# Optimization experiments

Measured on AMD Instinct MI355X. Metric: run time of the kernel, lower is better.

The kernel has to match this reference:

```python
import jax, jax.numpy as jnp
import numpy as np

N, E, G, H, L = 50000, 400000, 2000, 128, 5
NPG = N // G  # 25 nodes per graph
EPS = 1e-5    # PNA std epsilon
D_LOG = 1.0   # avg_d['log'] as in 3DInfomax PNAGNN


def setup_inputs():
    key = jax.random.key(0)
    ks = jax.random.split(key, 32)
    node_feat = jax.random.randint(ks[0], (N, 9), 0, 16)
    edge_feat = jax.random.randint(ks[1], (E, 3), 0, 5)
    src = jax.random.randint(ks[2], (E,), 0, N)
    off = jax.random.randint(ks[3], (E,), 1, NPG)
    # dst stays in the same graph as src and differs from src
    dst = (src // NPG) * NPG + (src % NPG + off) % NPG
    graph_id = jnp.arange(N) // NPG
    inp = dict(node_feat=node_feat, edge_feat=edge_feat, src=src, dst=dst,
               graph_id=graph_id)
    shapes = [("aemb_f", (144, H)), ("bemb_f", (15, H)),
              ("w_pre_f", (L, 3 * H, H)), ("b_pre_f", (L, H)),
              ("w_post_f", (L, 13 * H, H)), ("b_post_f", (L, H)),
              ("w_out3", (3 * H, 256)), ("b_out3", (256,)),
              ("aemb", (144, H)), ("bemb", (15, H)),
              ("w_pre", (L, 3 * H, H)), ("b_pre", (L, H)),
              ("w_post", (L, 13 * H, H)), ("b_post", (L, H)),
              ("w1", (3 * H + 256, H)), ("b1", (H,)),
              ("w2", (H, 128)), ("b2", (128,))]
    for i, (n, s) in enumerate(shapes):
        inp[n] = jax.random.normal(ks[4 + i], s, dtype=jnp.float32) * 0.05
    return inp


def _embed(table, x, vocab):
    # sum of per-feature embeddings (OGB Atom/Bond encoder)
    idx = x + jnp.arange(x.shape[1]) * vocab
    return table[idx].sum(axis=1)


def _pna_gnn(aemb, bemb, w_pre, b_pre, w_post, b_post,
             node_feat, edge_feat, src, dst):
    h = _embed(aemb, node_feat, 16)   # [N, H]
    e = _embed(bemb, edge_feat, 5)    # [E, H]
    deg = jax.ops.segment_sum(jnp.ones((src.shape[0],), jnp.float32), dst, N)
    safe_deg = jnp.maximum(deg, 1.0)[:, None]
    log_deg = jnp.log(deg + 1.0)[:, None]
    amp = log_deg / D_LOG                                   # amplification scaler
    att = jnp.where(log_deg > 0, D_LOG / jnp.where(log_deg > 0, log_deg, 1.0), 0.0)
    has_in = (deg > 0)[:, None]
    for l in range(L):
        h_in = h
        # pretrans over edges: cat(src, dst, edge) -> linear (pretrans_layers=1, last_activation='none')
        z = jnp.concatenate([h[src], h[dst], e], axis=-1) @ w_pre[l] + b_pre[l]  # [E, H]
        s1 = jax.ops.segment_sum(z, dst, N)
        mean = s1 / safe_deg
        mean_sq = jax.ops.segment_sum(z * z, dst, N) / safe_deg
        std = jnp.sqrt(jax.nn.relu(mean_sq - mean * mean) + EPS)
        mx = jnp.where(has_in, jax.ops.segment_max(z, dst, N), 0.0)
        mn = jnp.where(has_in, jax.ops.segment_min(z, dst, N), 0.0)
        agg = jnp.concatenate([mean, mx, mn, std], axis=-1)          # [N, 4H]
        f = jnp.concatenate([agg, agg * amp, agg * att], axis=-1)    # [N, 12H]
        f = jnp.where(has_in, f, 0.0)  # DGL leaves zero-in-degree nodes at zero
        h = jnp.concatenate([h, f], axis=-1) @ w_post[l] + b_post[l]
        h = h + h_in  # residual
    return h


def _readout(h, graph_id):
    mean = jax.ops.segment_sum(h, graph_id, G) / NPG
    mx = jax.ops.segment_max(h, graph_id, G)
    mn = jax.ops.segment_min(h, graph_id, G)
    return jnp.concatenate([mn, mx, mean], axis=-1)  # order: min, max, mean


def reference(aemb_f, bemb_f, w_pre_f, b_pre_f, w_post_f, b_post_f,
              w_out3, b_out3, aemb, bemb, w_pre, b_pre, w_post, b_post,
              w1, b1, w2, b2, node_feat, edge_feat, src, dst, graph_id):
    # frozen 3D branch (torch.no_grad + detach -> stop_gradient)
    h3 = _pna_gnn(aemb_f, bemb_f, w_pre_f, b_pre_f, w_post_f, b_post_f,
                  node_feat, edge_feat, src, dst)
    r3 = _readout(h3, graph_id)
    latent3d = jax.lax.stop_gradient(r3 @ w_out3 + b_out3)  # [G, 256]
    # trainable 2D branch
    h2 = _pna_gnn(aemb, bemb, w_pre, b_pre, w_post, b_post,
                  node_feat, edge_feat, src, dst)
    r2 = _readout(h2, graph_id)                              # [G, 384]
    x = jnp.concatenate([r2, latent3d], axis=-1)             # [G, 640]
    h1 = jax.nn.relu(x @ w1 + b1)
    return h1 @ w2 + b2                                      # [G, 128]
```

## Files before the change

kernel.cpp:

```cpp
#include <hip/hip_runtime.h>
#include <hip/hip_bf16.h>
#include <math.h>

#define Nn 50000
#define Ee 400000
#define Gg 2000
#define NPGc 25
#define Hc 128
#define Lc 5
#define M2c 50048
#define R2c 100096

typedef __attribute__((ext_vector_type(8))) short short8;
typedef __attribute__((ext_vector_type(4))) float fx4;

__device__ inline short bf16r(float x){
  unsigned u = __float_as_uint(x);
  unsigned r = (u + 0x7fffu + ((u >> 16) & 1u)) >> 16;
  return (short)r;
}
__device__ inline float bf16f(short s){
  return __uint_as_float(((unsigned)(unsigned short)s) << 16);
}

__global__ void deg_kernel(const int* __restrict__ dst, int* __restrict__ deg, int E){
  int i = blockIdx.x * blockDim.x + threadIdx.x;
  if (i < E) atomicAdd(&deg[dst[i]], 1);
}

__global__ void scan1_kernel(const int* __restrict__ deg, int* __restrict__ part,
                             int* __restrict__ bsums, int n){
  __shared__ int tmp[1024];
  int b = blockIdx.x, t = threadIdx.x;
  int i = b * 1024 + t;
  int v = (i < n) ? deg[i] : 0;
  tmp[t] = v;
  __syncthreads();
  for (int off = 1; off < 1024; off <<= 1){
    int add = (t >= off) ? tmp[t - off] : 0;
    __syncthreads();
    tmp[t] += add;
    __syncthreads();
  }
  part[i] = tmp[t];
  if (t == 1023) bsums[b] = tmp[1023];
}
__global__ void scan2_kernel(int* __restrict__ bsums, int nb){
  if (threadIdx.x == 0){
    int s = 0;
    for (int i = 0; i < nb; i++){ s += bsums[i]; bsums[i] = s; }
  }
}
__global__ void scan3_kernel(const int* __restrict__ part, const int* __restrict__ bsums,
                             int* __restrict__ rowstart, int n){
  int i = blockIdx.x * blockDim.x + threadIdx.x;
  if (i == 0) rowstart[0] = 0;
  if (i < n){
    int b = i >> 10;
    int base = b ? bsums[b - 1] : 0;
    rowstart[i + 1] = part[i] + base;
  }
}

__global__ void copy_int_kernel(const int* __restrict__ a, int* __restrict__ b, int n){
  int i = blockIdx.x * blockDim.x + threadIdx.x;
  if (i < n) b[i] = a[i];
}

__global__ void scatter_kernel(const int* __restrict__ src, const int* __restrict__ dst,
                               const int* __restrict__ ef, int* cursor,
                               int* __restrict__ pk_srt, int E){
  int i = blockIdx.x * blockDim.x + threadIdx.x;
  if (i >= E) return;
  int p = atomicAdd(&cursor[dst[i]], 1);
  int code = ef[i * 3 + 0] * 25 + ef[i * 3 + 1] * 5 + ef[i * 3 + 2];
  pk_srt[p] = (code << 16) | (src[i] % NPGc);
}

__global__ void ampatt_kernel(const int* __restrict__ deg, float* __restrict__ amp,
                              float* __restrict__ att, int n){
  int i = blockIdx.x * blockDim.x + threadIdx.x;
  if (i >= n) return;
  if (i >= Nn){ amp[i] = 0.f; att[i] = 0.f; return; }
  float d = (float)deg[i];
  float ld = logf(d + 1.0f);
  amp[i] = ld;
  att[i] = (deg[i] > 0) ? (1.0f / ld) : 0.0f;
}

__global__ void embed2_kernel(const int* __restrict__ nf,
                              const float* __restrict__ aemb_f,
                              const float* __restrict__ aemb_t,
                              float* __restrict__ h, short* __restrict__ h16){
  int idx = blockIdx.x * blockDim.x + threadIdx.x;
  if (idx >= R2c * Hc) return;
  int n = idx >> 7, c = idx & 127;
  int br = n >= M2c;
  int local = n - br * M2c;
  if (local >= Nn){ h[idx] = 0.f; h16[idx] = 0; return; }
  const float* aemb = br ? aemb_t : aemb_f;
  float s = 0.f;
#pragma unroll
  for (int f = 0; f < 9; f++){
    int row = nf[local * 9 + f] + 16 * f;
    s += aemb[row * Hc + c];
  }
  h[idx] = s;
  h16[idx] = bf16r(s);
}

__global__ void bsum2_kernel(const float* __restrict__ bemb_f, const float* __restrict__ bemb_t,
                             float* __restrict__ bsum2){
  int idx = blockIdx.x * blockDim.x + threadIdx.x;
  if (idx >= 2 * 125 * Hc) return;
  int b = idx / (125 * Hc);
  int rem = idx % (125 * Hc);
  int code = rem >> 7, c = rem & 127;
  int e0 = code / 25, e1 = (code / 5) % 5, e2 = code % 5;
  const float* bemb = b ? bemb_t : bemb_f;
  bsum2[idx] = bemb[e0 * Hc + c] + bemb[(5 + e1) * Hc + c] + bemb[(10 + e2) * Hc + c];
}

__global__ void conv_pre_all_kernel(const float* __restrict__ wpre_f,
                                    const float* __restrict__ wpre_t,
                                    short* __restrict__ btpre_all){
  int idx = blockIdx.x * blockDim.x + threadIdx.x;
  if (idx >= 2 * Lc * 256 * 128) return;
  int bl = idx / (256 * 128);
  int rem = idx % (256 * 128);
  int col = rem >> 7, k = rem & 127;
  int b = bl / Lc, l = bl % Lc;
  const float* wl = (b ? wpre_t : wpre_f) + (size_t)l * 384 * 128;
  float v = (col < 128) ? wl[k * 128 + col] : wl[(128 + k) * 128 + (col - 128)];
  btpre_all[(size_t)bl * 256 * 128 + col * 128 + k] = bf16r(v);
}
__global__ void conv_post_all_kernel(const float* __restrict__ wpost_f,
                                     const float* __restrict__ wpost_t,
                                     short* __restrict__ btpost_all){
  int idx = blockIdx.x * blockDim.x + threadIdx.x;
  if (idx >= 2 * Lc * 1664 * 128) return;
  int bl = idx / (1664 * 128);
  int rem = idx % (1664 * 128);
  int k = rem >> 7, c = rem & 127;
  int b = bl / Lc, l = bl % Lc;
  const float* wl = (b ? wpost_t : wpost_f) + (size_t)l * 1664 * 128;
  btpost_all[(size_t)bl * 128 * 1664 + (size_t)c * 1664 + k] = bf16r(wl[(size_t)k * 128 + c]);
}

__global__ void ezt_all_kernel(const float* __restrict__ wpre_f, const float* __restrict__ wpre_t,
                               const float* __restrict__ bpre_f, const float* __restrict__ bpre_t,
                               const float* __restrict__ bsum2, short* __restrict__ ezt16_all){
  int code = blockIdx.x;
  int bl   = blockIdx.y;
  int t = threadIdx.x;
  int b = bl / Lc, l = bl % Lc;
  const float* wl = (b ? wpre_t : wpre_f) + (size_t)l * 384 * 128 + 256 * 128;
  const float* bp = (b ? bpre_t : bpre_f) + (size_t)l * 128;
  __shared__ float bs[128];
  bs[t] = bsum2[((size_t)b * 125 + code) * 128 + t];
  __syncthreads();
  float acc = bp[t];
#pragma unroll 8
  for (int k = 0; k < 128; k++) acc += bs[k] * wl[k * 128 + t];
  ezt16_all[((size_t)bl * 125 + code) * 128 + t] = bf16r(acc);
}

__global__ void readout2_kernel(const float* __restrict__ h,
                                float* __restrict__ r3, float* __restrict__ r2){
  int bi = blockIdx.x;
  int br = bi >= Gg;
  int g = bi - br * Gg;
  int c = threadIdx.x;
  float mn = 3.402823466e38f, mx = -3.402823466e38f, s = 0.f;
  const float* hp = h + ((size_t)br * M2c + (size_t)g * NPGc) * Hc + c;
#pragma unroll
  for (int i = 0; i < NPGc; i++){
    float v = hp[i * Hc];
    mn = fminf(mn, v); mx = fmaxf(mx, v); s += v;
  }
  float* r = br ? r2 : r3;
  r[(size_t)g * 384 + c]       = mn;
  r[(size_t)g * 384 + 128 + c] = mx;
  r[(size_t)g * 384 + 256 + c] = s * (1.0f / NPGc);
}

__global__ __launch_bounds__(256)
void head_kernel(const float* __restrict__ r2, const float* __restrict__ r3,
                 const float* __restrict__ w_out3, const float* __restrict__ b_out3,
                 const float* __restrict__ w1, const float* __restrict__ b1,
                 const float* __restrict__ w2, const float* __restrict__ b2,
                 float* __restrict__ out)
{
  __shared__ float r3_s[384];
  __shared__ float x_s[640];
  __shared__ float h1_s[128];
  __shared__ float partial[256];
  int g = blockIdx.x, t = threadIdx.x;

  for (int i = t; i < 384; i += 256){
    float v2 = r2[(size_t)g * 384 + i];
    r3_s[i] = r3[(size_t)g * 384 + i];
    x_s[i] = v2;
  }
  __syncthreads();

  {
    float acc = b_out3[t];
#pragma unroll 8
    for (int k = 0; k < 384; k++) acc += r3_s[k] * w_out3[k * 256 + t];
    x_s[384 + t] = acc;
  }
  __syncthreads();

  {
    int c = t & 127, half = t >> 7;
    float acc = half ? 0.f : b1[c];
    int kb = half * 320;
#pragma unroll 8
    for (int k = kb; k < kb + 320; k++) acc += x_s[k] * w1[k * 128 + c];
    partial[t] = acc;
  }
  __syncthreads();
  if (t < 128) h1_s[t] = fmaxf(partial[t] + partial[t + 128], 0.f);
  __syncthreads();

  {
    int c = t & 127, half = t >> 7;
    float acc = half ? 0.f : b2[c];
    int kb = half * 64;
#pragma unroll 8
    for (int k = kb; k < kb + 64; k++) acc += h1_s[k] * w2[k * 128 + c];
    partial[t] = acc;
  }
  __syncthreads();
  if (t < 128) out[(size_t)g * 128 + t] = partial[t] + partial[t + 128];
}

__global__ __launch_bounds__(256, 4)
void fgemm_agg_kernel(const short* __restrict__ h16b,
                      const short* __restrict__ Bt,
                      const int* __restrict__ ez16,
                      const int* __restrict__ pk_srt, const int* __restrict__ rowstart,
                      short* __restrict__ aggOut)
{
  __shared__ short h_s[32 * 128];
  __shared__ short hsd_s[32 * 256];

  int tid = threadIdx.x;
  int g = blockIdx.x;
  int base = g * NPGc;

  {
    const int* src = (const int*)(h16b + (size_t)base * 128);
    int* dst = (int*)h_s;
    for (int t = tid; t < NPGc * 64; t += 256){
      int row = t >> 6, ci = t & 63;
      dst[row * 64 + (ci ^ ((row & 7) << 2))] = src[t];
    }
  }
  __syncthreads();

  int wv = tid >> 6, ln = tid & 63;
  int l15 = ln & 15, lq = ln >> 4;
  {
    fx4 acc[2][4];
#pragma unroll
    for (int mt = 0; mt < 2; mt++)
#pragma unroll
      for (int ct = 0; ct < 4; ct++) acc[mt][ct] = (fx4){0.f, 0.f, 0.f, 0.f};

    short8 af[2][4];
#pragma unroll
    for (int mt = 0; mt < 2; mt++){
      int row = mt * 16 + l15;
#pragma unroll
      for (int ks = 0; ks < 4; ks++){
        int sk = ks * 32 + lq * 8;
        af[mt][ks] = *(const short8*)(h_s + row * 128 + (sk ^ ((row & 7) << 3)));
      }
    }
#pragma unroll
    for (int ks = 0; ks < 4; ks++){
#pragma unroll
      for (int ct = 0; ct < 4; ct++){
        int col = wv * 64 + ct * 16 + l15;
        short8 bf = *(const short8*)(Bt + (size_t)col * 128 + ks * 32 + lq * 8);
        acc[0][ct] = __builtin_amdgcn_mfma_f32_16x16x32_bf16(af[0][ks], bf, acc[0][ct], 0, 0, 0);
        acc[1][ct] = __builtin_amdgcn_mfma_f32_16x16x32_bf16(af[1][ks], bf, acc[1][ct], 0, 0, 0);
      }
    }
#pragma unroll
    for (int mt = 0; mt < 2; mt++){
#pragma unroll
      for (int ct = 0; ct < 4; ct++){
        int cc = wv * 64 + ct * 16 + l15;
#pragma unroll
        for (int r = 0; r < 4; r++){
          int row = mt * 16 + lq * 4 + r;
          hsd_s[row * 256 + (cc ^ ((row & 7) << 3))] = bf16r(acc[mt][ct][r]);
        }
      }
    }
  }
  __syncthreads();

  int sub = tid & 15;
  int go = sub * 4;
  const int* hsd_i = (const int*)hsd_s;

#pragma unroll
  for (int rnd = 0; rnd < 2; rnd++){
    int nd = rnd * 16 + (tid >> 4);
    if (nd >= NPGc) continue;
    int node = base + nd;
    int e0 = rowstart[node], e1 = rowstart[node + 1];
    short* o = aggOut + (size_t)node * 512 + sub * 8;
    if (e1 <= e0){
      short8 z = {0, 0, 0, 0, 0, 0, 0, 0};
      *(short8*)(o)       = z;
      *(short8*)(o + 128) = z;
      *(short8*)(o + 256) = z;
      *(short8*)(o + 384) = z;
      continue;
    }

    float hdv[8];
    {
      int4 hd = *(const int4*)(hsd_i + nd * 128 + ((64 + go) ^ ((nd & 7) << 2)));
      const int* hp = (const int*)&hd;
#pragma unroll
      for (int i = 0; i < 4; i++){
        hdv[2 * i]     = __uint_as_float(((unsigned)hp[i]) << 16);
        hdv[2 * i + 1] = __uint_as_float(((unsigned)hp[i]) & 0xffff0000u);
      }
    }

    float sum[8], sq[8], mx[8], mn[8];
#pragma unroll
    for (int j = 0; j < 8; j++){
      sum[j] = 0.f; sq[j] = 0.f;
      mx[j] = -3.402823466e38f; mn[j] = 3.402823466e38f;
    }

    for (int k = e0; k < e1; k += 4){
      int pk[4];
#pragma unroll
      for (int t2 = 0; t2 < 4; t2++){
        int kk = (k + t2 < e1) ? (k + t2) : (e1 - 1);
        pk[t2] = pk_srt[kk];
      }
      int4 ev[4], hv[4];
#pragma unroll
      for (int t2 = 0; t2 < 4; t2++){
        int s = pk[t2] & 0xffff;
        ev[t2] = *(const int4*)(ez16 + (pk[t2] >> 16) * 64 + go);
        hv[t2] = *(const int4*)(hsd_i + s * 128 + (go ^ ((s & 7) << 2)));
      }
#pragma unroll
      for (int t2 = 0; t2 < 4; t2++){
        if (k + t2 < e1){
          const int* pp = (const int*)&hv[t2];
          const int* ee = (const int*)&ev[t2];
#pragma unroll
          for (int i = 0; i < 4; i++){
            float z0 = __uint_as_float(((unsigned)pp[i]) << 16) + hdv[2 * i]
                     + __uint_as_float(((unsigned)ee[i]) << 16);
            float z1 = __uint_as_float(((unsigned)pp[i]) & 0xffff0000u) + hdv[2 * i + 1]
                     + __uint_as_float(((unsigned)ee[i]) & 0xffff0000u);
            sum[2 * i] += z0;     sq[2 * i] += z0 * z0;
            mx[2 * i] = fmaxf(mx[2 * i], z0); mn[2 * i] = fminf(mn[2 * i], z0);
            sum[2 * i + 1] += z1; sq[2 * i + 1] += z1 * z1;
            mx[2 * i + 1] = fmaxf(mx[2 * i + 1], z1); mn[2 * i + 1] = fminf(mn[2 * i + 1], z1);
          }
        }
      }
    }

    float d = (float)(e1 - e0);
    float rd = 1.0f / d;
    short8 sm, sx, sn, sd;
#pragma unroll
    for (int j = 0; j < 8; j++){
      float m = sum[j] * rd;
      float v = sq[j] * rd - m * m; v = v > 0.f ? v : 0.f;
      sm[j] = bf16r(m);
      sx[j] = bf16r(mx[j]);
      sn[j] = bf16r(mn[j]);
      sd[j] = bf16r(sqrtf(v + 1e-5f));
    }
    *(short8*)(o)       = sm;
    *(short8*)(o + 128) = sx;
    *(short8*)(o + 256) = sn;
    *(short8*)(o + 384) = sd;
  }
}

__global__ __launch_bounds__(256, 4)
void post_gemm_kernel(const short* __restrict__ A16,
                      const short* __restrict__ aggG,
                      const short* __restrict__ Bt0, const short* __restrict__ Bt1,
                      const float* __restrict__ bias0, const float* __restrict__ bias1,
                      const float* __restrict__ amp, const float* __restrict__ att,
                      const float* __restrict__ resid,
                      float* __restrict__ C, short* __restrict__ C16)
{
  __shared__ short8 As[1024];
  __shared__ short8 Bs[1024];

  int tid = threadIdx.x;
  int row0 = blockIdx.x * 128;
  int br = row0 >= M2c;
  const short* Bt = br ? Bt1 : Bt0;
  const float* bias = br ? bias1 : bias0;
  int wv = tid >> 6, ln = tid & 63;
  int lo = ln & 15, q = ln >> 4;

  int a_rq = (tid >> 6) & 3, a_q = (tid >> 4) & 3, a_lo = tid & 15;
  int b_q = (tid >> 4) & 3, b_lo = tid & 15, b_ct0 = (tid >> 6) & 3;

  int arow[2]; float ampv[2], attv[2];
#pragma unroll
  for (int j = 0; j < 2; j++){
    arow[j] = row0 + (a_rq + 4 * j) * 16 + a_lo;
    int lr = arow[j] - br * M2c;
    ampv[j] = amp[lr]; attv[j] = att[lr];
  }
  int colb[2];
#pragma unroll
  for (int j = 0; j < 2; j++) colb[j] = ((b_ct0 + 4 * j) * 16 + b_lo) * 1664;

  fx4 acc[2][8];
#pragma unroll
  for (int j = 0; j < 2; j++)
#pragma unroll
    for (int ct = 0; ct < 8; ct++) acc[j][ct] = (fx4){0.f, 0.f, 0.f, 0.f};

  short8 ra[2][2], rb[2][2];
  auto loadA = [&](int s){
    if (s < 2){
#pragma unroll
      for (int i = 0; i < 2; i++){
        int k = s * 64 + i * 32 + a_q * 8;
#pragma unroll
        for (int j = 0; j < 2; j++)
          ra[i][j] = *(const short8*)(A16 + (size_t)arow[j] * 128 + k);
      }
    } else {
      int kc = (s - 2) / 3;
#pragma unroll
      for (int i = 0; i < 2; i++){
        int koff = kc * 64 + i * 32 + a_q * 8;
#pragma unroll
        for (int j = 0; j < 2; j++)
          ra[i][j] = *(const short8*)(aggG + (size_t)arow[j] * 512 + koff);
      }
    }
  };
  auto loadB = [&](int s){
    int gkb;
    if (s < 2) gkb = s * 64;
    else {
      int t = s - 2, kc = t / 3, ph = t % 3;
      gkb = (ph == 0 ? 128 : (ph == 1 ? 640 : 1152)) + kc * 64;
    }
#pragma unroll
    for (int i = 0; i < 2; i++){
      int gk = gkb + i * 32 + b_q * 8;
#pragma unroll
      for (int j = 0; j < 2; j++)
        rb[i][j] = *(const short8*)(Bt + (size_t)colb[j] + gk);
    }
  };

  loadA(0); loadB(0);
  for (int s = 0; s < 26; s++){
    int ph = (s < 2) ? 0 : (s - 2) % 3;
    __syncthreads();
    if (ph == 0){
#pragma unroll
      for (int i = 0; i < 2; i++)
#pragma unroll
        for (int j = 0; j < 2; j++) As[i * 512 + j * 256 + tid] = ra[i][j];
    } else {
#pragma unroll
      for (int i = 0; i < 2; i++)
#pragma unroll
        for (int j = 0; j < 2; j++){
          float sc = (ph == 1) ? ampv[j] : attv[j];
          short8 v = ra[i][j];
#pragma unroll
          for (int e = 0; e < 8; e++)
            ((short*)&v)[e] = bf16r(bf16f(((short*)&v)[e]) * sc);
          As[i * 512 + j * 256 + tid] = v;
        }
    }
#pragma unroll
    for (int i = 0; i < 2; i++)
#pragma unroll
      for (int j = 0; j < 2; j++) Bs[i * 512 + j * 256 + tid] = rb[i][j];
    __syncthreads();
    if (s < 25){
      loadB(s + 1);
      if (s + 1 < 2 || (s - 1) % 3 == 0) loadA(s + 1);
    }
    short8 a00 = As[wv * 64 + ln];
    short8 a10 = As[512 + wv * 64 + ln];
    short8 a01 = As[256 + wv * 64 + ln];
    short8 a11 = As[768 + wv * 64 + ln];
#pragma unroll
    for (int ct = 0; ct < 8; ct++){
      short8 b0 = Bs[ct * 64 + ln];
      short8 b1 = Bs[512 + ct * 64 + ln];
      acc[0][ct] = __builtin_amdgcn_mfma_f32_16x16x32_bf16(a00, b0, acc[0][ct], 0, 0, 0);
      acc[0][ct] = __builtin_amdgcn_mfma_f32_16x16x32_bf16(a10, b1, acc[0][ct], 0, 0, 0);
      acc[1][ct] = __builtin_amdgcn_mfma_f32_16x16x32_bf16(a01, b0, acc[1][ct], 0, 0, 0);
      acc[1][ct] = __builtin_amdgcn_mfma_f32_16x16x32_bf16(a11, b1, acc[1][ct], 0, 0, 0);
    }
  }

#pragma unroll
  for (int j = 0; j < 2; j++){
#pragma unroll
    for (int ct = 0; ct < 8; ct++){
      int col = ct * 16 + lo;
      float bcol = bias[col];
#pragma unroll
      for (int r = 0; r < 4; r++){
        int row = row0 + (wv + 4 * j) * 16 + q * 4 + r;
        float v = acc[j][ct][r] + bcol + resid[(size_t)row * 128 + col];
        C[(size_t)row * 128 + col] = v;
        C16[(size_t)row * 128 + col] = bf16r(v);
      }
    }
  }
}

extern "C" void kernel_launch(void* const* d_in, const int* in_sizes, int n_in,
                              void* d_out, int out_size, void* d_ws, size_t ws_size,
                              hipStream_t stream)
{
  const int*   node_feat = (const int*)  d_in[0];
  const int*   edge_feat = (const int*)  d_in[1];
  const int*   src       = (const int*)  d_in[2];
  const int*   dst       = (const int*)  d_in[3];
  const float* aemb_f  = (const float*) d_in[5];
  const float* bemb_f  = (const float*) d_in[6];
  const float* w_pre_f = (const float*) d_in[7];
  const float* b_pre_f = (const float*) d_in[8];
  const float* w_post_f= (const float*) d_in[9];
  const float* b_post_f= (const float*) d_in[10];
  const float* w_out3  = (const float*) d_in[11];
  const float* b_out3  = (const float*) d_in[12];
  const float* aemb    = (const float*) d_in[13];
  const float* bemb    = (const float*) d_in[14];
  const float* w_pre   = (const float*) d_in[15];
  const float* b_pre   = (const float*) d_in[16];
  const float* w_post  = (const float*) d_in[17];
  const float* b_post  = (const float*) d_in[18];
  const float* w1      = (const float*) d_in[19];
  const float* b1      = (const float*) d_in[20];
  const float* w2      = (const float*) d_in[21];
  const float* b2      = (const float*) d_in[22];
  float* out = (float*)d_out;

  char* w = (char*)d_ws;
  auto carve = [&](size_t bytes) -> void* {
    void* p = (void*)w;
    w += (bytes + 255) & ~(size_t)255;
    return p;
  };
  float* h         = (float*)carve((size_t)R2c * Hc * 4);
  short* h16       = (short*)carve((size_t)R2c * Hc * 2);
  short* aggG      = (short*)carve((size_t)R2c * 512 * 2);
  short* btpre_all = (short*)carve((size_t)2 * Lc * 256 * 128 * 2);
  short* btpost_all= (short*)carve((size_t)2 * Lc * 128 * 1664 * 2);
  short* ezt16_all = (short*)carve((size_t)2 * Lc * 125 * Hc * 2);
  float* amp       = (float*)carve((size_t)M2c * 4);
  float* att       = (float*)carve((size_t)M2c * 4);
  int* rowstart = (int*)carve((size_t)(Nn + 1) * 4);
  int* pk_srt   = (int*)carve((size_t)Ee * 4);

  char* ali = (char*)aggG;
  float* r3     = (float*)(ali);
  float* r2     = (float*)(ali + (size_t)4 * 1024 * 1024);
  int*   deg    = (int*)  (ali + (size_t)8 * 1024 * 1024);
  int*   cursor = (int*)  (ali + (size_t)9 * 1024 * 1024);
  int*   part   = (int*)  (ali + (size_t)10 * 1024 * 1024);
  int*   bsums  = (int*)  (ali + (size_t)11 * 1024 * 1024);
  float* bsum2  = (float*)(ali + (size_t)12 * 1024 * 1024);

  hipMemsetAsync(deg, 0, (size_t)Nn * 4, stream);
  deg_kernel<<<(Ee + 255) / 256, 256, 0, stream>>>(dst, deg, Ee);
  scan1_kernel<<<49, 1024, 0, stream>>>(deg, part, bsums, Nn);
  scan2_kernel<<<1, 64, 0, stream>>>(bsums, 49);
  scan3_kernel<<<(Nn + 255) / 256, 256, 0, stream>>>(part, bsums, rowstart, Nn);
  copy_int_kernel<<<(Nn + 255) / 256, 256, 0, stream>>>(rowstart, cursor, Nn);
  scatter_kernel<<<(Ee + 255) / 256, 256, 0, stream>>>(src, dst, edge_feat, cursor,
                                                       pk_srt, Ee);
  ampatt_kernel<<<(M2c + 255) / 256, 256, 0, stream>>>(deg, amp, att, M2c);

  hipMemsetAsync(aggG + (size_t)Nn * 512, 0, (size_t)(M2c - Nn) * 512 * 2, stream);
  hipMemsetAsync(aggG + ((size_t)M2c + Nn) * 512, 0, (size_t)(M2c - Nn) * 512 * 2, stream);

  bsum2_kernel<<<(2 * 125 * Hc + 255) / 256, 256, 0, stream>>>(bemb_f, bemb, bsum2);
  conv_pre_all_kernel<<<(2 * Lc * 256 * 128 + 255) / 256, 256, 0, stream>>>(
      w_pre_f, w_pre, btpre_all);
  conv_post_all_kernel<<<(2 * Lc * 1664 * 128 + 255) / 256, 256, 0, stream>>>(
      w_post_f, w_post, btpost_all);
  ezt_all_kernel<<<dim3(125, 2 * Lc), 128, 0, stream>>>(
      w_pre_f, w_pre, b_pre_f, b_pre, bsum2, ezt16_all);

  embed2_kernel<<<(R2c * Hc + 255) / 256, 256, 0, stream>>>(
      node_feat, aemb_f, aemb, h, h16);

  for (int l = 0; l < Lc; l++){
    const short* pre0 = btpre_all + (size_t)(0 * Lc + l) * 256 * 128;
    const short* pre1 = btpre_all + (size_t)(1 * Lc + l) * 256 * 128;
    const short* post0 = btpost_all + (size_t)(0 * Lc + l) * 128 * 1664;
    const short* post1 = btpost_all + (size_t)(1 * Lc + l) * 128 * 1664;
    const int* ez0 = (const int*)(ezt16_all + (size_t)(0 * Lc + l) * 125 * Hc);
    const int* ez1 = (const int*)(ezt16_all + (size_t)(1 * Lc + l) * 125 * Hc);
    const float* bp0 = b_post_f + (size_t)l * 128;
    const float* bp1 = b_post   + (size_t)l * 128;

    fgemm_agg_kernel<<<Gg, 256, 0, stream>>>(
        h16, pre0, ez0, pk_srt, rowstart, aggG);
    fgemm_agg_kernel<<<Gg, 256, 0, stream>>>(
        h16 + (size_t)M2c * 128, pre1, ez1, pk_srt, rowstart,
        aggG + (size_t)M2c * 512);

    post_gemm_kernel<<<R2c / 128, 256, 0, stream>>>(
        h16, aggG, post0, post1, bp0, bp1, amp, att, h, h, h16);
  }

  readout2_kernel<<<2 * Gg, 128, 0, stream>>>(h, r3, r2);
  head_kernel<<<Gg, 256, 0, stream>>>(r2, r3, w_out3, b_out3, w1, b1, w2, b2, out);
}
```

Measured before the change: 1.379 ms.

## Merge branch fgemm launches, split post GEMM by column halves with double-buffered h16

The two per-branch fgemm_agg launches become one launch of 2*Gg blocks that pick their branch from the block index. post_gemm now splits the 128 output columns into two 64-column blocks on a 2D grid, which doubles the block count (about 782 to 1564) and halves per-block accumulators and B staging. Since column halves would otherwise race on h16 (read as A and written as output), h16 is double-buffered and swapped each layer. The A operand and its amp/att scaling are now loaded and computed twice, once per column half.

```diff
diff --git a/kernel.cpp b/kernel.cpp
--- a/kernel.cpp
+++ b/kernel.cpp
@@ -237,17 +237,23 @@
 }
 
 __global__ __launch_bounds__(256, 4)
-void fgemm_agg_kernel(const short* __restrict__ h16b,
-                      const short* __restrict__ Bt,
-                      const int* __restrict__ ez16,
+void fgemm_agg_kernel(const short* __restrict__ h16,
+                      const short* __restrict__ pre0, const short* __restrict__ pre1,
+                      const int* __restrict__ ez0, const int* __restrict__ ez1,
                       const int* __restrict__ pk_srt, const int* __restrict__ rowstart,
-                      short* __restrict__ aggOut)
+                      short* __restrict__ aggG)
 {
   __shared__ short h_s[32 * 128];
   __shared__ short hsd_s[32 * 256];
 
   int tid = threadIdx.x;
-  int g = blockIdx.x;
+  int bi = blockIdx.x;
+  int brn = bi >= Gg;
+  int g = bi - brn * Gg;
+  const short* h16b = h16 + (size_t)brn * M2c * 128;
+  const short* Bt = brn ? pre1 : pre0;
+  const int* ez16 = brn ? ez1 : ez0;
+  short* aggOut = aggG + (size_t)brn * M2c * 512;
   int base = g * NPGc;
 
   {
@@ -405,10 +411,11 @@
                       float* __restrict__ C, short* __restrict__ C16)
 {
   __shared__ short8 As[1024];
-  __shared__ short8 Bs[1024];
+  __shared__ short8 Bs[512];
 
   int tid = threadIdx.x;
-  int row0 = blockIdx.x * 128;
+  int row0 = blockIdx.y * 128;
+  int col0 = blockIdx.x * 64;
   int br = row0 >= M2c;
   const short* Bt = br ? Bt1 : Bt0;
   const float* bias = br ? bias1 : bias0;
@@ -416,7 +423,7 @@
   int lo = ln & 15, q = ln >> 4;
 
   int a_rq = (tid >> 6) & 3, a_q = (tid >> 4) & 3, a_lo = tid & 15;
-  int b_q = (tid >> 4) & 3, b_lo = tid & 15, b_ct0 = (tid >> 6) & 3;
+  int b_q = (tid >> 4) & 3, b_lo = tid & 15, b_ct = (tid >> 6) & 3;
 
   int arow[2]; float ampv[2], attv[2];
 #pragma unroll
@@ -425,17 +432,15 @@
     int lr = arow[j] - br * M2c;
     ampv[j] = amp[lr]; attv[j] = att[lr];
   }
-  int colb[2];
-#pragma unroll
-  for (int j = 0; j < 2; j++) colb[j] = ((b_ct0 + 4 * j) * 16 + b_lo) * 1664;
-
-  fx4 acc[2][8];
+  size_t colb = (size_t)(col0 + b_ct * 16 + b_lo) * 1664;
+
+  fx4 acc[2][4];
 #pragma unroll
   for (int j = 0; j < 2; j++)
 #pragma unroll
-    for (int ct = 0; ct < 8; ct++) acc[j][ct] = (fx4){0.f, 0.f, 0.f, 0.f};
-
-  short8 ra[2][2], rb[2][2];
+    for (int ct = 0; ct < 4; ct++) acc[j][ct] = (fx4){0.f, 0.f, 0.f, 0.f};
+
+  short8 ra[2][2], rb[2];
   auto loadA = [&](int s){
     if (s < 2){
 #pragma unroll
@@ -464,12 +469,8 @@
       gkb = (ph == 0 ? 128 : (ph == 1 ? 640 : 1152)) + kc * 64;
     }
 #pragma unroll
-    for (int i = 0; i < 2; i++){
-      int gk = gkb + i * 32 + b_q * 8;
-#pragma unroll
-      for (int j = 0; j < 2; j++)
-        rb[i][j] = *(const short8*)(Bt + (size_t)colb[j] + gk);
-    }
+    for (int i = 0; i < 2; i++)
+      rb[i] = *(const short8*)(Bt + colb + gkb + i * 32 + b_q * 8);
   };
 
   loadA(0); loadB(0);
@@ -495,9 +496,7 @@
         }
     }
 #pragma unroll
-    for (int i = 0; i < 2; i++)
-#pragma unroll
-      for (int j = 0; j < 2; j++) Bs[i * 512 + j * 256 + tid] = rb[i][j];
+    for (int i = 0; i < 2; i++) Bs[i * 256 + tid] = rb[i];
     __syncthreads();
     if (s < 25){
       loadB(s + 1);
@@ -508,9 +507,9 @@
     short8 a01 = As[256 + wv * 64 + ln];
     short8 a11 = As[768 + wv * 64 + ln];
 #pragma unroll
-    for (int ct = 0; ct < 8; ct++){
+    for (int ct = 0; ct < 4; ct++){
       short8 b0 = Bs[ct * 64 + ln];
-      short8 b1 = Bs[512 + ct * 64 + ln];
+      short8 b1 = Bs[256 + ct * 64 + ln];
       acc[0][ct] = __builtin_amdgcn_mfma_f32_16x16x32_bf16(a00, b0, acc[0][ct], 0, 0, 0);
       acc[0][ct] = __builtin_amdgcn_mfma_f32_16x16x32_bf16(a10, b1, acc[0][ct], 0, 0, 0);
       acc[1][ct] = __builtin_amdgcn_mfma_f32_16x16x32_bf16(a01, b0, acc[1][ct], 0, 0, 0);
@@ -521,8 +520,8 @@
 #pragma unroll
   for (int j = 0; j < 2; j++){
 #pragma unroll
-    for (int ct = 0; ct < 8; ct++){
-      int col = ct * 16 + lo;
+    for (int ct = 0; ct < 4; ct++){
+      int col = col0 + ct * 16 + lo;
       float bcol = bias[col];
 #pragma unroll
       for (int r = 0; r < 4; r++){
@@ -570,7 +569,8 @@
     return p;
   };
   float* h         = (float*)carve((size_t)R2c * Hc * 4);
-  short* h16       = (short*)carve((size_t)R2c * Hc * 2);
+  short* h16_a     = (short*)carve((size_t)R2c * Hc * 2);
+  short* h16_b     = (short*)carve((size_t)R2c * Hc * 2);
   short* aggG      = (short*)carve((size_t)R2c * 512 * 2);
   short* btpre_all = (short*)carve((size_t)2 * Lc * 256 * 128 * 2);
   short* btpost_all= (short*)carve((size_t)2 * Lc * 128 * 1664 * 2);
@@ -610,8 +610,10 @@
   ezt_all_kernel<<<dim3(125, 2 * Lc), 128, 0, stream>>>(
       w_pre_f, w_pre, b_pre_f, b_pre, bsum2, ezt16_all);
 
+  short* g_cur = h16_a;
+  short* g_nxt = h16_b;
   embed2_kernel<<<(R2c * Hc + 255) / 256, 256, 0, stream>>>(
-      node_feat, aemb_f, aemb, h, h16);
+      node_feat, aemb_f, aemb, h, g_cur);
 
   for (int l = 0; l < Lc; l++){
     const short* pre0 = btpre_all + (size_t)(0 * Lc + l) * 256 * 128;
@@ -623,14 +625,13 @@
     const float* bp0 = b_post_f + (size_t)l * 128;
     const float* bp1 = b_post   + (size_t)l * 128;
 
-    fgemm_agg_kernel<<<Gg, 256, 0, stream>>>(
-        h16, pre0, ez0, pk_srt, rowstart, aggG);
-    fgemm_agg_kernel<<<Gg, 256, 0, stream>>>(
-        h16 + (size_t)M2c * 128, pre1, ez1, pk_srt, rowstart,
-        aggG + (size_t)M2c * 512);
-
-    post_gemm_kernel<<<R2c / 128, 256, 0, stream>>>(
-        h16, aggG, post0, post1, bp0, bp1, amp, att, h, h, h16);
+    fgemm_agg_kernel<<<2 * Gg, 256, 0, stream>>>(
+        g_cur, pre0, pre1, ez0, ez1, pk_srt, rowstart, aggG);
+
+    post_gemm_kernel<<<dim3(2, R2c / 128), 256, 0, stream>>>(
+        g_cur, aggG, post0, post1, bp0, bp1, amp, att, h, h, g_nxt);
+
+    { short* t = g_cur; g_cur = g_nxt; g_nxt = t; }
   }
 
   readout2_kernel<<<2 * Gg, 128, 0, stream>>>(h, r3, r2);
```

After: 1.202 ms. -12.8%, faster.
